# Optimization experiments

Measured on AMD Instinct MI355X. Metric: run time of the kernel, lower is better.

The kernel has to match this reference:

```python
import jax, jax.numpy as jnp
import numpy as np

B, N, D, H, L = 32, 576, 768, 8, 2
HD = D // H            # head_dim = 96
MLP = 4 * D            # 3072
GRID = 24              # sqrt(576), == max_positions
MP = 24                # max_positions
SD = 64                # spatial_dim
EPS = 1e-5


def _ln(x, g, b):
    m = jnp.mean(x, axis=-1, keepdims=True)
    v = jnp.mean((x - m) ** 2, axis=-1, keepdims=True)
    return (x - m) * jax.lax.rsqrt(v + EPS) * g + b


def setup_inputs() -> dict:
    key = jax.random.key(0)
    ks = jax.random.split(key, 16)
    s = 0.02
    inp = {
        "x": jax.random.normal(ks[0], (B, N, D), jnp.float32),
        # spatial position encoding params
        "row_embed": jax.random.normal(ks[1], (MP, SD // 2), jnp.float32) * s,
        "col_embed": jax.random.normal(ks[2], (MP, SD // 2), jnp.float32) * s,
        "pos_w": jax.random.normal(ks[3], (SD, D), jnp.float32) * s,
        "pos_b": jnp.zeros((D,), jnp.float32),
        "rel_bias": jax.random.normal(ks[4], (2 * MP - 1, 2 * MP - 1), jnp.float32) * s,
        # per-layer params, stacked on leading L axis
        "ln1_g": jnp.ones((L, D), jnp.float32),
        "ln1_b": jnp.zeros((L, D), jnp.float32),
        "ln2_g": jnp.ones((L, D), jnp.float32),
        "ln2_b": jnp.zeros((L, D), jnp.float32),
        "Wq": jax.random.normal(ks[5], (L, D, D), jnp.float32) * s,
        "bq": jnp.zeros((L, D), jnp.float32),
        "Wk": jax.random.normal(ks[6], (L, D, D), jnp.float32) * s,
        "bk": jnp.zeros((L, D), jnp.float32),
        "Wv": jax.random.normal(ks[7], (L, D, D), jnp.float32) * s,
        "bv": jnp.zeros((L, D), jnp.float32),
        "Wo": jax.random.normal(ks[8], (L, D, D), jnp.float32) * s,
        "bo": jnp.zeros((L, D), jnp.float32),
        "W1": jax.random.normal(ks[9], (L, D, MLP), jnp.float32) * s,
        "b1": jnp.zeros((L, MLP), jnp.float32),
        "W2": jax.random.normal(ks[10], (L, MLP, D), jnp.float32) * s,
        "b2": jnp.zeros((L, D), jnp.float32),
    }
    return inp


def reference(x, row_embed, col_embed, pos_w, pos_b, rel_bias,
              ln1_g, ln1_b, ln2_g, ln2_b,
              Wq, bq, Wk, bk, Wv, bv, Wo, bo,
              W1, b1, W2, b2):
    scale = HD ** -0.5

    # ---- absolute 2D position encoding (N = GRID*GRID, no CLS) ----
    pe = jnp.concatenate([
        jnp.broadcast_to(row_embed[:, None, :], (GRID, GRID, SD // 2)),
        jnp.broadcast_to(col_embed[None, :, :], (GRID, GRID, SD // 2)),
    ], axis=-1).reshape(N, SD)                      # [N, SD]
    x = x + (pe @ pos_w + pos_b)                    # broadcast over B

    # ---- relative position bias [N, N] ----
    coords = jnp.stack(jnp.meshgrid(jnp.arange(GRID), jnp.arange(GRID),
                                    indexing="ij")).reshape(2, N)  # [2, N]
    rel = coords[:, :, None] - coords[:, None, :]   # [2, N, N]
    idx = (rel[0] + MP - 1) * (2 * MP - 1) + (rel[1] + MP - 1)
    bias = rel_bias.reshape(-1)[idx]                # [N, N]

    # ---- reasoning layers ----
    for l in range(L):
        n1 = _ln(x, ln1_g[l], ln1_b[l])
        q = (n1 @ Wq[l] + bq[l]).reshape(B, N, H, HD)
        k = (n1 @ Wk[l] + bk[l]).reshape(B, N, H, HD)
        v = (n1 @ Wv[l] + bv[l]).reshape(B, N, H, HD)
        scores = jnp.einsum("bnhd,bmhd->bhnm", q, k) * scale + bias
        attn = jax.nn.softmax(scores, axis=-1)
        out = jnp.einsum("bhnm,bmhd->bnhd", attn, v).reshape(B, N, D)
        x = x + (out @ Wo[l] + bo[l])
        n2 = _ln(x, ln2_g[l], ln2_b[l])
        h = jax.nn.gelu(n2 @ W1[l] + b1[l], approximate=False)
        x = x + (h @ W2[l] + b2[l])
    return x
```

## Files before the change

### kernel.cpp

```cpp
#include <hip/hip_runtime.h>
#include <hip/hip_bf16.h>
#include <cstdint>
#include <cstddef>

typedef unsigned short u16;
using frag  = __attribute__((ext_vector_type(8))) short;
using f32x4 = __attribute__((ext_vector_type(4))) float;

#define DEV __device__ __forceinline__

DEV float bf2f(u16 u) { union { unsigned int i; float f; } x; x.i = ((unsigned int)u) << 16; return x.f; }
DEV u16 f2bf(float f) {
  union { float f; unsigned int i; } x; x.f = f;
  unsigned int r = x.i + 0x7fffu + ((x.i >> 16) & 1u);
  return (u16)(r >> 16);
}

#define MFMA16(a, b, c) __builtin_amdgcn_mfma_f32_16x16x32_bf16((a), (b), (c), 0, 0, 0)

DEV void cp16_g2l(const u16* g, u16* l) {
  __builtin_amdgcn_global_load_lds(
      reinterpret_cast<const __attribute__((address_space(1))) unsigned int*>(
          reinterpret_cast<uintptr_t>(g)),
      reinterpret_cast<__attribute__((address_space(3))) unsigned int*>(
          reinterpret_cast<uintptr_t>(l)),
      16, 0, 0);
}

template<int N> DEV void waitvm() {
  if constexpr (N == 0)      asm volatile("s_waitcnt vmcnt(0)" ::: "memory");
  else if constexpr (N == 3) asm volatile("s_waitcnt vmcnt(3)" ::: "memory");
  else if constexpr (N == 4) asm volatile("s_waitcnt vmcnt(4)" ::: "memory");
  else if constexpr (N == 6) asm volatile("s_waitcnt vmcnt(6)" ::: "memory");
  else if constexpr (N == 8) asm volatile("s_waitcnt vmcnt(8)" ::: "memory");
}

DEV void phase_barrier() {
  asm volatile("" ::: "memory");
  __builtin_amdgcn_sched_barrier(0);
  __builtin_amdgcn_s_barrier();
  __builtin_amdgcn_sched_barrier(0);
  asm volatile("" ::: "memory");
}

#define SB   32
#define SN   576
#define SD_  768
#define SH   8
#define SHD  96
#define SMLP 3072
#define BN_  (SB * SN)
#define IMG  (SN * SD_)
#define QKVS 2304

#define P_RE   0
#define P_CE   768
#define P_PW   1536
#define P_PB   50688
#define P_REL  51456
#define P_L1G  53696
#define P_L1B  55232
#define P_L2G  56768
#define P_L2B  58304
#define P_BQ   59840
#define P_BK   61376
#define P_BV   62912
#define P_BO   64448
#define P_B1   65984
#define P_B2   72128
#define P_FQB  73664
#define P_TOT  78272

__global__ void detect_kernel(const void* probe, int* flag) {
  if (threadIdx.x == 0 && blockIdx.x == 0) {
    unsigned int w = *(const unsigned int*)probe;
    flag[0] = (w == 0x3F800000u) ? 1 : 0;
  }
}

__global__ void canon_params(const void* re, const void* ce, const void* pw, const void* pb,
                             const void* rel, const void* l1g, const void* l1b,
                             const void* l2g, const void* l2b,
                             const void* pbq, const void* pbk, const void* pbv, const void* pbo,
                             const void* pb1, const void* pb2,
                             u16* __restrict__ P, const int* __restrict__ flag) {
  int i = blockIdx.x * 256 + threadIdx.x;
  const void* src; int si;
  if      (i < 768)     { src = re;  si = i; }
  else if (i < 1536)    { src = ce;  si = i - 768; }
  else if (i < 50688)   { src = pw;  si = i - 1536; }
  else if (i < 51456)   { src = pb;  si = i - 50688; }
  else if (i < 53665)   { src = rel; si = i - 51456; }
  else if (i < P_L1G)   { return; }
  else if (i < P_L1B)   { src = l1g; si = i - P_L1G; }
  else if (i < P_L2G)   { src = l1b; si = i - P_L1B; }
  else if (i < P_L2B)   { src = l2g; si = i - P_L2G; }
  else if (i < P_BQ)    { src = l2b; si = i - P_L2B; }
  else if (i < P_BK)    { src = pbq; si = i - P_BQ; }
  else if (i < P_BV)    { src = pbk; si = i - P_BK; }
  else if (i < P_BO)    { src = pbv; si = i - P_BV; }
  else if (i < P_B1)    { src = pbo; si = i - P_BO; }
  else if (i < P_B2)    { src = pb1; si = i - P_B1; }
  else if (i < P_FQB)   { src = pb2; si = i - P_B2; }
  else if (i < P_TOT) {
    int j = i - P_FQB, l = j / 2304, c = j % 2304;
    src = (c < 768) ? pbq : (c < 1536 ? pbk : pbv);
    si = l * 768 + (c % 768);
  }
  else return;
  P[i] = flag[0] ? f2bf(((const float*)src)[si]) : ((const u16*)src)[si];
}

__global__ void posenc_kernel(const u16* __restrict__ P, float* __restrict__ pe) {
  int n = blockIdx.x;
  int r = n / 24, c = n % 24;
  const u16* re = P + P_RE;
  const u16* ce = P + P_CE;
  const u16* pw = P + P_PW;
  const u16* pb = P + P_PB;
  for (int d = threadIdx.x; d < SD_; d += 256) {
    float acc = bf2f(pb[d]);
    for (int s = 0; s < 32; ++s) {
      acc += bf2f(re[r * 32 + s]) * bf2f(pw[s * SD_ + d]);
      acc += bf2f(ce[c * 32 + s]) * bf2f(pw[(32 + s) * SD_ + d]);
    }
    pe[n * SD_ + d] = acc;
  }
}

__global__ void bias_kernel(const u16* __restrict__ P, float* __restrict__ biasT) {
  int i = blockIdx.x * 256 + threadIdx.x;
  if (i < SN * SN) {
    int qi = i / SN, kj = i % SN;
    int ri = qi / 24, ci = qi % 24, rj = kj / 24, cj = kj % 24;
    int idx = (ri - rj + 23) * 47 + (ci - cj + 23);
    biasT[i] = bf2f(P[P_REL + idx]);
  }
}

__global__ void xinit_kernel(const void* __restrict__ xin, const float* __restrict__ pe,
                             float* __restrict__ X, const int* __restrict__ flag) {
  int idx = (blockIdx.x * 256 + threadIdx.x) * 4;
  int b = blockIdx.y;
  float vx, vy, vz, vw;
  if (flag[0]) {
    float4 t = *(const float4*)((const float*)xin + (size_t)b * IMG + idx);
    vx = t.x; vy = t.y; vz = t.z; vw = t.w;
  } else {
    ushort4 t = *(const ushort4*)((const u16*)xin + (size_t)b * IMG + idx);
    vx = bf2f(t.x); vy = bf2f(t.y); vz = bf2f(t.z); vw = bf2f(t.w);
  }
  float4 p = *(const float4*)(pe + idx);
  float4 o;
  o.x = vx + p.x; o.y = vy + p.y; o.z = vz + p.z; o.w = vw + p.w;
  *(float4*)(X + (size_t)b * IMG + idx) = o;
}

__global__ void transpose_any(const void* __restrict__ W, size_t eOff,
                              u16* __restrict__ Wt, int K, int N,
                              const int* __restrict__ flag) {
  __shared__ u16 tile[64][65];
  const int fp32 = flag[0];
  int n0 = blockIdx.x * 64, k0 = blockIdx.y * 64;
  int tx = threadIdx.x, ty = threadIdx.y;
#pragma unroll
  for (int j = 0; j < 16; ++j) {
    int k = ty + 4 * j;
    size_t si = eOff + (size_t)(k0 + k) * N + n0 + tx;
    tile[k][tx] = fp32 ? f2bf(((const float*)W)[si]) : ((const u16*)W)[si];
  }
  __syncthreads();
#pragma unroll
  for (int j = 0; j < 16; ++j) {
    int n = ty + 4 * j;
    Wt[(size_t)(n0 + n) * K + k0 + tx] = tile[tx][n];
  }
}

__global__ __launch_bounds__(256) void ln_kernel(const float* __restrict__ X,
                                                 const u16* __restrict__ g,
                                                 const u16* __restrict__ bb,
                                                 u16* __restrict__ Outn) {
  int row = blockIdx.x * 4 + (threadIdx.x >> 6);
  int lane = threadIdx.x & 63;
  const float* xr = X + (size_t)row * SD_;
  float4 v[3];
  float s = 0.f, sq = 0.f;
#pragma unroll
  for (int i = 0; i < 3; ++i) {
    v[i] = *(const float4*)(xr + i * 256 + lane * 4);
    s += v[i].x + v[i].y + v[i].z + v[i].w;
    sq += v[i].x * v[i].x + v[i].y * v[i].y + v[i].z * v[i].z + v[i].w * v[i].w;
  }
#pragma unroll
  for (int o = 1; o < 64; o <<= 1) {
    s += __shfl_xor(s, o, 64);
    sq += __shfl_xor(sq, o, 64);
  }
  float mean = s * (1.0f / 768.0f);
  float var = sq * (1.0f / 768.0f) - mean * mean;
  float rstd = rsqrtf(fmaxf(var, 0.f) + 1e-5f);
  u16* orow = Outn + (size_t)row * SD_;
#pragma unroll
  for (int i = 0; i < 3; ++i) {
    int d = i * 256 + lane * 4;
    ushort4 gv = *(const ushort4*)(g + d);
    ushort4 bv = *(const ushort4*)(bb + d);
    ushort4 ov;
    ov.x = f2bf((v[i].x - mean) * rstd * bf2f(gv.x) + bf2f(bv.x));
    ov.y = f2bf((v[i].y - mean) * rstd * bf2f(gv.y) + bf2f(bv.y));
    ov.z = f2bf((v[i].z - mean) * rstd * bf2f(gv.z) + bf2f(bv.z));
    ov.w = f2bf((v[i].w - mean) * rstd * bf2f(gv.w) + bf2f(bv.w));
    *(ushort4*)(orow + d) = ov;
  }
}

template<int MREP, int MODE>
__global__ __launch_bounds__(512, 2) void gemm256(
    const u16* __restrict__ A, const u16* __restrict__ Bt,
    const u16* __restrict__ bias, u16* __restrict__ Out,
    float* __restrict__ Xres, int Ncols, int K) {
  constexpr int BM = MREP * 32;
  constexpr int ASLOT = BM * 32;
  constexpr int BSLOT = 256 * 32;
  constexpr int LPT = (BM == 256) ? 4 : 3;
  __shared__ __align__(1024) u16 sA[4 * ASLOT];
  __shared__ __align__(1024) u16 sB[4 * BSLOT];

  const int tid = threadIdx.x;
  const int lane = tid & 63;
  const int w = tid >> 6;
  const int wm = w >> 2, wn = w & 3;
  const int m16 = lane & 15, q4 = lane >> 4;

  int bn, bm;
  {
    const int gx = gridDim.x;
    const int nwg = gx * gridDim.y;
    const int l = blockIdx.y * gx + blockIdx.x;
    const int q = nwg >> 3, r = nwg & 7;
    const int xcd = l & 7, idx = l >> 3;
    const int base = (xcd < r) ? xcd * (q + 1) : r * (q + 1) + (xcd - r) * q;
    const int wg = base + idx;
    bn = wg % gx;
    bm = wg / gx;
  }
  const int nt = K >> 5;

  const int srow = tid >> 2;
  const int kcol = (((tid & 3) ^ ((tid >> 3) & 3)) << 3);
  const u16* Ag = A + (size_t)(bm * BM + srow) * K + kcol;
  const u16* Bg = Bt + (size_t)(bn * 256 + srow) * K + kcol;
  const size_t rstep = (size_t)128 * K;
  u16* const Adst = sA + tid * 8;
  u16* const Bdst = sB + tid * 8;

  const int xk = ((q4 ^ ((m16 >> 1) & 3)) << 4);
  const char* const aBase = (const char*)sA + (((wm * (BM / 2) + m16) << 6) + xk);
  const char* const bBase = (const char*)sB + (((wn * 64 + m16) << 6) + xk);

  f32x4 acc[MREP][4] = {};

  auto stage_a = [&](int t) {
    const int s = t & 3;
    cp16_g2l(Ag + (size_t)t * 32, Adst + s * ASLOT);
    if constexpr (BM == 256) cp16_g2l(Ag + (size_t)t * 32 + rstep, Adst + s * ASLOT + 4096);
  };
  auto stage_b = [&](int t) {
    const int s = t & 3;
    cp16_g2l(Bg + (size_t)t * 32, Bdst + s * BSLOT);
    cp16_g2l(Bg + (size_t)t * 32 + rstep, Bdst + s * BSLOT + 4096);
  };

  if (nt > 0) { stage_a(0); stage_b(0); }
  if (nt > 1) { stage_a(1); stage_b(1); }
  if (nt > 2) { stage_a(2); stage_b(2); }
  if (nt > 2) waitvm<2 * LPT>(); else waitvm<0>();
  phase_barrier();

  for (int t = 0; t < nt; ++t) {
    const int s = t & 3;
    const bool st = (t + 3) < nt;
    const char* const aS = aBase + s * (ASLOT * 2);
    const char* const bS = bBase + s * (BSLOT * 2);
    frag bf[4], af[4];
#pragma unroll
    for (int j = 0; j < 4; ++j) bf[j] = *(const frag*)(bS + j * 1024);
#pragma unroll
    for (int i = 0; i < 4; ++i) af[i] = *(const frag*)(aS + i * 1024);
    if (st) stage_a(t + 3);
    if constexpr (MREP == 4) {
      if (st) stage_b(t + 3);
      if (t < nt - 3) waitvm<6>();
      else if (t == nt - 3) waitvm<3>();
      else if (t == nt - 2) waitvm<0>();
    }
    phase_barrier();
    __builtin_amdgcn_s_setprio(1);
#pragma unroll
    for (int i = 0; i < 4; ++i)
#pragma unroll
      for (int j = 0; j < 4; ++j) acc[i][j] = MFMA16(af[i], bf[j], acc[i][j]);
    __builtin_amdgcn_s_setprio(0);
    if constexpr (MREP == 8) {
      frag a2[4];
#pragma unroll
      for (int i = 0; i < 4; ++i) a2[i] = *(const frag*)(aS + 4096 + i * 1024);
      if (st) stage_b(t + 3);
      if (t < nt - 3) waitvm<8>();
      else if (t == nt - 3) waitvm<4>();
      else if (t == nt - 2) waitvm<0>();
      phase_barrier();
      __builtin_amdgcn_s_setprio(1);
#pragma unroll
      for (int i = 0; i < 4; ++i)
#pragma unroll
        for (int j = 0; j < 4; ++j) acc[4 + i][j] = MFMA16(a2[i], bf[j], acc[4 + i][j]);
      __builtin_amdgcn_s_setprio(0);
    }
  }

  const int col0 = bn * 256 + wn * 64;
  float bcol[4];
#pragma unroll
  for (int j = 0; j < 4; ++j) bcol[j] = bf2f(bias[col0 + j * 16 + m16]);

  if constexpr (MODE == 2) {
#pragma unroll
    for (int i = 0; i < MREP; ++i) {
      const int row0 = bm * BM + wm * (BM / 2) + i * 16 + q4 * 4;
#pragma unroll
      for (int j = 0; j < 4; ++j)
#pragma unroll
        for (int r = 0; r < 4; ++r)
          Xres[(size_t)(row0 + r) * Ncols + col0 + j * 16 + m16] += acc[i][j][r] + bcol[j];
    }
  } else {
    __syncthreads();
    u16* const wls = sA + w * 2048;
    const int lr = lane >> 3, lc = (lane & 7) * 8;
#pragma unroll
    for (int i = 0; i < MREP; ++i) {
#pragma unroll
      for (int j = 0; j < 4; ++j)
#pragma unroll
        for (int r = 0; r < 4; ++r) {
          float v = acc[i][j][r] + bcol[j];
          if constexpr (MODE == 1) v = 0.5f * v * (1.0f + erff(v * 0.70710678118654752f));
          wls[(q4 * 4 + r) * 72 + j * 16 + m16] = f2bf(v);
        }
      asm volatile("s_waitcnt lgkmcnt(0)" ::: "memory");
      frag o0 = *(const frag*)(wls + lr * 72 + lc);
      frag o1 = *(const frag*)(wls + (lr + 8) * 72 + lc);
      const size_t gr0 = (size_t)(bm * BM + wm * (BM / 2) + i * 16 + lr);
      *(frag*)(Out + gr0 * Ncols + col0 + lc) = o0;
      *(frag*)(Out + (gr0 + 8) * Ncols + col0 + lc) = o1;
    }
  }
}

__global__ __launch_bounds__(256, 2) void attn_flash(const u16* __restrict__ QKV,
                                                     const float* __restrict__ biasT,
                                                     u16* __restrict__ Out, int b0) {
  __shared__ __align__(16) u16 Ks[64 * 104];
  __shared__ __align__(16) u16 Vt[96 * 72];
  __shared__ __align__(16) u16 Ps[64 * 72];
  const int tid = threadIdx.x, lane = tid & 63, w = tid >> 6;
  const int m16 = lane & 15, q4 = lane >> 4;
  const int qt = blockIdx.x, h = blockIdx.y, bl = blockIdx.z;
  const int q0 = qt * 64;
  const int row0 = bl * SN;
  const float scale = 0.10206207261596575f;

  int skey[3], soff[3];
#pragma unroll
  for (int u = 0; u < 3; ++u) { int c = tid + u * 256; skey[u] = c / 12; soff[u] = (c % 12) * 8; }

  frag aq[3];
  {
    const u16* qptr = QKV + (size_t)(row0 + q0 + w * 16 + m16) * QKVS + h * SHD;
#pragma unroll
    for (int ks = 0; ks < 3; ++ks) aq[ks] = *(const frag*)(qptr + ks * 32 + q4 * 8);
  }

  f32x4 oacc[6] = {};
  float mrun[4], lrun[4];
#pragma unroll
  for (int r = 0; r < 4; ++r) { mrun[r] = -1e30f; lrun[r] = 0.f; }

  uint4 kreg[3], vreg[3];
  auto loadK = [&](int kt) {
#pragma unroll
    for (int u = 0; u < 3; ++u)
      kreg[u] = *(const uint4*)(QKV + (size_t)(row0 + kt * 64 + skey[u]) * QKVS + 768 + h * SHD + soff[u]);
  };
  auto loadV = [&](int kt) {
#pragma unroll
    for (int u = 0; u < 3; ++u)
      vreg[u] = *(const uint4*)(QKV + (size_t)(row0 + kt * 64 + skey[u]) * QKVS + 1536 + h * SHD + soff[u]);
  };
  auto writeKV = [&]() {
#pragma unroll
    for (int u = 0; u < 3; ++u) {
      *(uint4*)(Ks + skey[u] * 104 + soff[u]) = kreg[u];
      u16 tmp[8]; *(uint4*)tmp = vreg[u];
#pragma unroll
      for (int j = 0; j < 8; ++j) {
        int d = soff[u] + j;
        Vt[d * 72 + (skey[u] ^ (((d >> 3) & 7) << 3))] = tmp[j];
      }
    }
  };

  loadK(0); loadV(0);
  writeKV();
  __syncthreads();

  for (int kt = 0; kt < 9; ++kt) {
    if (kt < 8) loadK(kt + 1);

    f32x4 sa[4];
    __builtin_amdgcn_s_setprio(1);
#pragma unroll
    for (int nt = 0; nt < 4; ++nt) {
      sa[nt] = (f32x4){0.f, 0.f, 0.f, 0.f};
#pragma unroll
      for (int ks = 0; ks < 3; ++ks) {
        frag bk = *(const frag*)(Ks + (nt * 16 + m16) * 104 + ks * 32 + q4 * 8);
        sa[nt] = MFMA16(aq[ks], bk, sa[nt]);
      }
    }
    __builtin_amdgcn_s_setprio(0);

    if (kt < 8) loadV(kt + 1);

    float sv[4][4], mnew[4];
#pragma unroll
    for (int r = 0; r < 4; ++r) {
      const float* brow = biasT + (size_t)(q0 + w * 16 + q4 * 4 + r) * SN + kt * 64;
      float mx = mrun[r];
#pragma unroll
      for (int nt = 0; nt < 4; ++nt) {
        float s = sa[nt][r] * scale + brow[nt * 16 + m16];
        sv[r][nt] = s;
        mx = fmaxf(mx, s);
      }
#pragma unroll
      for (int o = 1; o < 16; o <<= 1) mx = fmaxf(mx, __shfl_xor(mx, o, 64));
      mnew[r] = mx;
    }
#pragma unroll
    for (int r = 0; r < 4; ++r) {
      float alpha = __expf(mrun[r] - mnew[r]);
      mrun[r] = mnew[r];
      float psum = 0.f;
#pragma unroll
      for (int nt = 0; nt < 4; ++nt) {
        float p = __expf(sv[r][nt] - mnew[r]);
        psum += p;
        Ps[(w * 16 + q4 * 4 + r) * 72 + nt * 16 + m16] = f2bf(p);
      }
#pragma unroll
      for (int o = 1; o < 16; o <<= 1) psum += __shfl_xor(psum, o, 64);
      lrun[r] = lrun[r] * alpha + psum;
#pragma unroll
      for (int dt = 0; dt < 6; ++dt) oacc[dt][r] *= alpha;
    }

    __builtin_amdgcn_s_setprio(1);
#pragma unroll
    for (int ch = 0; ch < 2; ++ch) {
      frag ap = *(const frag*)(Ps + (w * 16 + m16) * 72 + ch * 32 + q4 * 8);
#pragma unroll
      for (int dt = 0; dt < 6; ++dt) {
        const int d = dt * 16 + m16;
        frag bv = *(const frag*)(Vt + d * 72 + ((ch * 32 + q4 * 8) ^ (((d >> 3) & 7) << 3)));
        oacc[dt] = MFMA16(ap, bv, oacc[dt]);
      }
    }
    __builtin_amdgcn_s_setprio(0);

    if (kt < 8) {
      __syncthreads();
      writeKV();
      __syncthreads();
    }
  }

#pragma unroll
  for (int r = 0; r < 4; ++r) {
    float inv = 1.0f / lrun[r];
    size_t obase = ((size_t)((b0 + bl) * SN + q0 + w * 16 + q4 * 4 + r)) * SD_ + h * SHD;
#pragma unroll
    for (int dt = 0; dt < 6; ++dt)
      Out[obase + dt * 16 + m16] = f2bf(oacc[dt][r] * inv);
  }
}

__global__ void castout_kernel(const float* __restrict__ X, void* __restrict__ out,
                               const int* __restrict__ flag) {
  int i = (blockIdx.x * 256 + threadIdx.x) * 4;
  float4 v = *(const float4*)(X + i);
  if (flag[0]) {
    *(float4*)((float*)out + i) = v;
  } else {
    ushort4 o;
    o.x = f2bf(v.x); o.y = f2bf(v.y); o.z = f2bf(v.z); o.w = f2bf(v.w);
    *(ushort4*)((u16*)out + i) = o;
  }
}

extern "C" void kernel_launch(void* const* d_in, const int* in_sizes, int n_in,
                              void* d_out, int out_size, void* d_ws, size_t ws_size,
                              hipStream_t stream) {
  const void* x_in      = d_in[0];
  const void* row_embed = d_in[1];
  const void* col_embed = d_in[2];
  const void* pos_w     = d_in[3];
  const void* pos_b     = d_in[4];
  const void* rel_bias  = d_in[5];
  const void* ln1_g = d_in[6];
  const void* ln1_b = d_in[7];
  const void* ln2_g = d_in[8];
  const void* ln2_b = d_in[9];
  const void* Wq = d_in[10];
  const void* bq = d_in[11];
  const void* Wk = d_in[12];
  const void* bk = d_in[13];
  const void* Wv = d_in[14];
  const void* bv = d_in[15];
  const void* Wo = d_in[16];
  const void* bo = d_in[17];
  const void* W1 = d_in[18];
  const void* b1 = d_in[19];
  const void* W2 = d_in[20];
  const void* b2 = d_in[21];

  const bool tierA = ws_size >= (size_t)131000000;
  const int BC = tierA ? 16 : 8;
  const int RC = tierA ? 9216 : 4608;
  const int mR = BC * SN;
  const size_t qkvB = (size_t)mR * QKVS * 2;
  size_t bigB = qkvB;
  { size_t hB = (size_t)RC * SMLP * 2; if (hB > bigB) bigB = hB; }

  char* ws = (char*)d_ws;
  size_t off = 0;
  auto alloc = [&](size_t bytes) -> void* {
    void* p = ws + off;
    off += (bytes + 255) & ~(size_t)255;
    return p;
  };

  int*   flag = (int*)alloc(256);
  float* X    = (float*)alloc((size_t)BN_ * SD_ * 4);
  char*  big  = (char*)alloc(bigB);
  u16* QKVc = (u16*)big;
  u16* Hbuf = (u16*)big;
  float* pe    = (float*)alloc((size_t)SN * SD_ * 4);
  float* biasT = (float*)alloc((size_t)SN * SN * 4);
  u16* P     = (u16*)alloc((size_t)P_TOT * 2 + 256);
  u16* WqkvT = (u16*)alloc((size_t)QKVS * SD_ * 2);
  u16* WoT   = (u16*)alloc((size_t)SD_ * SD_ * 2);
  u16* W1T   = (u16*)alloc((size_t)SD_ * SMLP * 2);
  u16* W2T   = (u16*)alloc((size_t)SMLP * SD_ * 2);
  u16* Nfull = (u16*)d_out;

  detect_kernel<<<1, 64, 0, stream>>>(ln1_g, flag);
  canon_params<<<(P_TOT + 255) / 256, 256, 0, stream>>>(
      row_embed, col_embed, pos_w, pos_b, rel_bias,
      ln1_g, ln1_b, ln2_g, ln2_b, bq, bk, bv, bo, b1, b2, P, flag);

  posenc_kernel<<<SN, 256, 0, stream>>>(P, pe);
  bias_kernel<<<(SN * SN + 255) / 256, 256, 0, stream>>>(P, biasT);
  xinit_kernel<<<dim3(IMG / 1024, SB), 256, 0, stream>>>(x_in, pe, X, flag);

  dim3 tb(64, 4);
  for (int l = 0; l < 2; ++l) {
    const size_t wOff = (size_t)l * SD_ * SD_;
    const size_t w1Off = (size_t)l * SD_ * SMLP;
    transpose_any<<<dim3(12, 12), tb, 0, stream>>>(Wq, wOff, WqkvT, SD_, SD_, flag);
    transpose_any<<<dim3(12, 12), tb, 0, stream>>>(Wk, wOff, WqkvT + SD_ * SD_, SD_, SD_, flag);
    transpose_any<<<dim3(12, 12), tb, 0, stream>>>(Wv, wOff, WqkvT + 2 * SD_ * SD_, SD_, SD_, flag);
    transpose_any<<<dim3(12, 12), tb, 0, stream>>>(Wo, wOff, WoT, SD_, SD_, flag);
    transpose_any<<<dim3(48, 12), tb, 0, stream>>>(W1, w1Off, W1T, SD_, SMLP, flag);
    transpose_any<<<dim3(12, 48), tb, 0, stream>>>(W2, w1Off, W2T, SMLP, SD_, flag);

    ln_kernel<<<BN_ / 4, 256, 0, stream>>>(X, P + P_L1G + l * SD_, P + P_L1B + l * SD_, Nfull);

    for (int c = 0; c < SB / BC; ++c) {
      const size_t r0 = (size_t)c * mR;
      gemm256<4, 0><<<dim3(QKVS / 256, mR / 128), 512, 0, stream>>>(
          Nfull + r0 * SD_, WqkvT, P + P_FQB + l * QKVS, QKVc, nullptr, QKVS, SD_);
      attn_flash<<<dim3(SN / 64, SH, BC), 256, 0, stream>>>(QKVc, biasT, Nfull, c * BC);
    }
    gemm256<4, 2><<<dim3(SD_ / 256, BN_ / 128), 512, 0, stream>>>(
        Nfull, WoT, P + P_BO + l * SD_, nullptr, X, SD_, SD_);

    ln_kernel<<<BN_ / 4, 256, 0, stream>>>(X, P + P_L2G + l * SD_, P + P_L2B + l * SD_, Nfull);

    for (int c = 0; c < BN_ / RC; ++c) {
      const size_t r0 = (size_t)c * RC;
      gemm256<8, 1><<<dim3(SMLP / 256, RC / 256), 512, 0, stream>>>(
          Nfull + r0 * SD_, W1T, P + P_B1 + l * SMLP, Hbuf, nullptr, SMLP, SD_);
      gemm256<4, 2><<<dim3(SD_ / 256, RC / 128), 512, 0, stream>>>(
          Hbuf, W2T, P + P_B2 + l * SD_, nullptr, X + r0 * SD_, SD_, SMLP);
    }
  }

  castout_kernel<<<(size_t)BN_ * SD_ / 1024, 256, 0, stream>>>(X, d_out, flag);
}
```

Baseline: 1.569 ms.

## Pre-transpose V and double-buffer K/V via async global-to-LDS copies in attention

Adds a separate kernel that transposes V into a per-head [HD, N] buffer, so the attention kernel can stage both K and V with direct global_load_lds copies into double-buffered, XOR-swizzled shared memory. This replaces the register round trip, the per-element V transpose scatter and the two barriers per iteration with a single barrier. The attention workgroups are also remapped across the 8 XCDs. The cost is an extra kernel launch, an extra pass over V through memory, more LDS per block, and dropping the 2-blocks-per-CU launch bound.

```diff
diff --git a/kernel.cpp b/kernel.cpp
--- a/kernel.cpp
+++ b/kernel.cpp
@@ -177,6 +177,32 @@
   }
 }
 
+__global__ __launch_bounds__(256) void vtrans_kernel(const u16* __restrict__ QKV,
+                                                     u16* __restrict__ VT) {
+  __shared__ u16 t[64 * 104];
+  const int tid = threadIdx.x;
+  const int kt = blockIdx.x, h = blockIdx.y, bl = blockIdx.z;
+  const size_t inbase = ((size_t)(bl * SN + kt * 64)) * QKVS + 1536 + h * SHD;
+#pragma unroll
+  for (int u = 0; u < 3; ++u) {
+    int c = tid + u * 256;
+    int key = c / 12, coff = c % 12;
+    *(uint4*)(t + key * 104 + coff * 8) =
+        *(const uint4*)(QKV + inbase + (size_t)key * QKVS + coff * 8);
+  }
+  __syncthreads();
+  u16* outb = VT + (size_t)(bl * SH + h) * SHD * SN + (size_t)kt * 64;
+#pragma unroll
+  for (int u = 0; u < 3; ++u) {
+    int c = tid + u * 256;
+    int d = c >> 3, coff = c & 7;
+    u16 tmp[8];
+#pragma unroll
+    for (int j = 0; j < 8; ++j) tmp[j] = t[(coff * 8 + j) * 104 + d];
+    *(uint4*)(outb + (size_t)d * SN + coff * 8) = *(uint4*)tmp;
+  }
+}
+
 __global__ __launch_bounds__(256) void ln_kernel(const float* __restrict__ X,
                                                  const u16* __restrict__ g,
                                                  const u16* __restrict__ bb,
@@ -359,23 +385,30 @@
   }
 }
 
-__global__ __launch_bounds__(256, 2) void attn_flash(const u16* __restrict__ QKV,
-                                                     const float* __restrict__ biasT,
-                                                     u16* __restrict__ Out, int b0) {
-  __shared__ __align__(16) u16 Ks[64 * 104];
-  __shared__ __align__(16) u16 Vt[96 * 72];
+__global__ __launch_bounds__(256) void attn_flash(const u16* __restrict__ QKV,
+                                                  const u16* __restrict__ VT,
+                                                  const float* __restrict__ biasT,
+                                                  u16* __restrict__ Out, int b0) {
+  __shared__ __align__(16) u16 Ks[2][64 * 96];
+  __shared__ __align__(16) u16 Vs[2][96 * 64];
   __shared__ __align__(16) u16 Ps[64 * 72];
   const int tid = threadIdx.x, lane = tid & 63, w = tid >> 6;
   const int m16 = lane & 15, q4 = lane >> 4;
-  const int qt = blockIdx.x, h = blockIdx.y, bl = blockIdx.z;
+  int qt, h, bl;
+  {
+    const int nx = gridDim.x;
+    const int nwg = nx * gridDim.y * gridDim.z;
+    const int l = (blockIdx.z * gridDim.y + blockIdx.y) * nx + blockIdx.x;
+    const int q = nwg >> 3, r = nwg & 7;
+    const int xcd = l & 7, idx = l >> 3;
+    const int base = (xcd < r) ? xcd * (q + 1) : r * (q + 1) + (xcd - r) * q;
+    const int wg = base + idx;
+    qt = wg % nx; int rest = wg / nx; h = rest % SH; bl = rest / SH;
+  }
   const int q0 = qt * 64;
   const int row0 = bl * SN;
   const float scale = 0.10206207261596575f;
 
-  int skey[3], soff[3];
-#pragma unroll
-  for (int u = 0; u < 3; ++u) { int c = tid + u * 256; skey[u] = c / 12; soff[u] = (c % 12) * 8; }
-
   frag aq[3];
   {
     const u16* qptr = QKV + (size_t)(row0 + q0 + w * 16 + m16) * QKVS + h * SHD;
@@ -383,41 +416,37 @@
     for (int ks = 0; ks < 3; ++ks) aq[ks] = *(const frag*)(qptr + ks * 32 + q4 * 8);
   }
 
+  const size_t kbase = (size_t)row0 * QKVS + 768 + h * SHD;
+  const u16* Vg = VT + (size_t)(bl * SH + h) * SHD * SN;
+  auto stage = [&](int kt) {
+    const int b = kt & 1;
+#pragma unroll
+    for (int u = 0; u < 3; ++u) {
+      const int c = tid + u * 256;
+      const int row = c / 12, coff = c % 12;
+      const int gc = (coff < 8) ? (coff ^ (row & 7)) : (8 | ((coff & 3) ^ (row & 3)));
+      cp16_g2l(QKV + kbase + (size_t)(kt * 64 + row) * QKVS + gc * 8, Ks[b] + c * 8);
+    }
+#pragma unroll
+    for (int u = 0; u < 3; ++u) {
+      const int c = tid + u * 256;
+      const int d = c >> 3, coff = c & 7;
+      const int gc = coff ^ (d & 7);
+      cp16_g2l(Vg + (size_t)d * SN + kt * 64 + gc * 8, Vs[b] + c * 8);
+    }
+  };
+
   f32x4 oacc[6] = {};
   float mrun[4], lrun[4];
 #pragma unroll
   for (int r = 0; r < 4; ++r) { mrun[r] = -1e30f; lrun[r] = 0.f; }
 
-  uint4 kreg[3], vreg[3];
-  auto loadK = [&](int kt) {
-#pragma unroll
-    for (int u = 0; u < 3; ++u)
-      kreg[u] = *(const uint4*)(QKV + (size_t)(row0 + kt * 64 + skey[u]) * QKVS + 768 + h * SHD + soff[u]);
-  };
-  auto loadV = [&](int kt) {
-#pragma unroll
-    for (int u = 0; u < 3; ++u)
-      vreg[u] = *(const uint4*)(QKV + (size_t)(row0 + kt * 64 + skey[u]) * QKVS + 1536 + h * SHD + soff[u]);
-  };
-  auto writeKV = [&]() {
-#pragma unroll
-    for (int u = 0; u < 3; ++u) {
-      *(uint4*)(Ks + skey[u] * 104 + soff[u]) = kreg[u];
-      u16 tmp[8]; *(uint4*)tmp = vreg[u];
-#pragma unroll
-      for (int j = 0; j < 8; ++j) {
-        int d = soff[u] + j;
-        Vt[d * 72 + (skey[u] ^ (((d >> 3) & 7) << 3))] = tmp[j];
-      }
-    }
-  };
-
-  loadK(0); loadV(0);
-  writeKV();
+  stage(0);
   __syncthreads();
 
   for (int kt = 0; kt < 9; ++kt) {
-    if (kt < 8) loadK(kt + 1);
+    const int b = kt & 1;
+    if (kt < 8) stage(kt + 1);
 
     f32x4 sa[4];
     __builtin_amdgcn_s_setprio(1);
@@ -426,13 +455,13 @@
       sa[nt] = (f32x4){0.f, 0.f, 0.f, 0.f};
 #pragma unroll
       for (int ks = 0; ks < 3; ++ks) {
-        frag bk = *(const frag*)(Ks + (nt * 16 + m16) * 104 + ks * 32 + q4 * 8);
+        const int ce = (ks < 2) ? (((ks * 4 + q4) ^ (m16 & 7)) * 8)
+                                : (256 + ((q4 ^ (m16 & 3)) * 8));
+        frag bk = *(const frag*)(Ks[b] + (nt * 16 + m16) * 96 + ce);
         sa[nt] = MFMA16(aq[ks], bk, sa[nt]);
       }
     }
     __builtin_amdgcn_s_setprio(0);
-
-    if (kt < 8) loadV(kt + 1);
 
     float sv[4][4], mnew[4];
 #pragma unroll
@@ -473,18 +502,14 @@
       frag ap = *(const frag*)(Ps + (w * 16 + m16) * 72 + ch * 32 + q4 * 8);
 #pragma unroll
       for (int dt = 0; dt < 6; ++dt) {
-        const int d = dt * 16 + m16;
-        frag bv = *(const frag*)(Vt + d * 72 + ((ch * 32 + q4 * 8) ^ (((d >> 3) & 7) << 3)));
+        frag bv = *(const frag*)(Vs[b] + (dt * 16 + m16) * 64 +
+                                 (((ch * 4 + q4) ^ (m16 & 7)) * 8));
         oacc[dt] = MFMA16(ap, bv, oacc[dt]);
       }
     }
     __builtin_amdgcn_s_setprio(0);
 
-    if (kt < 8) {
-      __syncthreads();
-      writeKV();
-      __syncthreads();
-    }
+    __syncthreads();
   }
 
 #pragma unroll
@@ -541,7 +566,8 @@
   const int RC = tierA ? 9216 : 4608;
   const int mR = BC * SN;
   const size_t qkvB = (size_t)mR * QKVS * 2;
-  size_t bigB = qkvB;
+  const size_t vtB  = (size_t)BC * SH * SHD * SN * 2;
+  size_t bigB = qkvB + vtB;
   { size_t hB = (size_t)RC * SMLP * 2; if (hB > bigB) bigB = hB; }
 
   char* ws = (char*)d_ws;
@@ -556,6 +582,7 @@
   float* X    = (float*)alloc((size_t)BN_ * SD_ * 4);
   char*  big  = (char*)alloc(bigB);
   u16* QKVc = (u16*)big;
+  u16* VTc  = QKVc + (size_t)mR * QKVS;
   u16* Hbuf = (u16*)big;
   float* pe    = (float*)alloc((size_t)SN * SD_ * 4);
   float* biasT = (float*)alloc((size_t)SN * SN * 4);
@@ -592,7 +619,8 @@
       const size_t r0 = (size_t)c * mR;
       gemm256<4, 0><<<dim3(QKVS / 256, mR / 128), 512, 0, stream>>>(
           Nfull + r0 * SD_, WqkvT, P + P_FQB + l * QKVS, QKVc, nullptr, QKVS, SD_);
-      attn_flash<<<dim3(SN / 64, SH, BC), 256, 0, stream>>>(QKVc, biasT, Nfull, c * BC);
+      vtrans_kernel<<<dim3(9, SH, BC), 256, 0, stream>>>(QKVc, VTc);
+      attn_flash<<<dim3(SN / 64, SH, BC), 256, 0, stream>>>(QKVc, VTc, biasT, Nfull, c * BC);
     }
     gemm256<4, 2><<<dim3(SD_ / 256, BN_ / 128), 512, 0, stream>>>(
         Nfull, WoT, P + P_BO + l * SD_, nullptr, X, SD_, SD_);
```

After: 1.495 ms. 4.7% less time.
